# Kernel optimization log

Measured on AMD Instinct MI355X. Metric: run time of the kernel, lower is better.

The kernel has to match this reference:

```python
import jax, jax.numpy as jnp
import numpy as np
from jax import lax

NUM_HEADS = 8
HEAD_DIM = 32  # filters_per_head


def conv1d_same(x, w, b):
    # x: [B, T, Cin], w: [K, Cin, Cout] (WIO), 'same' padding, stride 1
    y = lax.conv_general_dilated(x, w, window_strides=(1,), padding='SAME',
                                 dimension_numbers=('NWC', 'WIO', 'NWC'))
    return y + b


def setup_inputs() -> dict:
    key = jax.random.key(0)
    ks = jax.random.split(key, 9)
    B, T, C = 8, 2048, 256
    K = 3
    s = 1.0 / np.sqrt(K * C)
    return {
        'x': jax.random.normal(ks[0], (B, T, C), dtype=jnp.float32),
        'Wq': jax.random.normal(ks[1], (K, C, C), dtype=jnp.float32) * s,
        'bq': jnp.zeros((C,), dtype=jnp.float32),
        'Wk': jax.random.normal(ks[2], (K, C, C), dtype=jnp.float32) * s,
        'bk': jnp.zeros((C,), dtype=jnp.float32),
        'Wv': jax.random.normal(ks[3], (K, C, C), dtype=jnp.float32) * s,
        'bv': jnp.zeros((C,), dtype=jnp.float32),
        'Wo': jax.random.normal(ks[4], (K, C, C), dtype=jnp.float32) * s,
        'bo': jnp.zeros((C,), dtype=jnp.float32),
    }


def reference(x, Wq, bq, Wk, bk, Wv, bv, Wo, bo):
    B, T, C = x.shape
    q = conv1d_same(x, Wq, bq)
    k = conv1d_same(x, Wk, bk)
    v = conv1d_same(x, Wv, bv)

    def split(t):  # [B, T, C] -> [B, H, T, D]
        return t.reshape(B, T, NUM_HEADS, HEAD_DIM).transpose(0, 2, 1, 3)

    q, k, v = split(q), split(k), split(v)
    scale = 1.0 / jnp.sqrt(jnp.float32(HEAD_DIM))
    logits = jnp.einsum('bhqd,bhkd->bhqk', q, k) * scale  # [B,H,T,T]
    attn = jax.nn.softmax(logits, axis=-1)
    ctx = jnp.einsum('bhqk,bhkd->bhqd', attn, v)
    ctx = ctx.transpose(0, 2, 1, 3).reshape(B, T, C)
    out = x + conv1d_same(ctx, Wo, bo)
    return out
```

## Files before the change

kernel.cpp:

```cpp
#include <hip/hip_runtime.h>
#include <math.h>

#define BDIM 8
#define TDIM 2048
#define CDIM 256
#define HDIM 8
#define DDIM 32
#define TP   (TDIM + 2)

typedef __attribute__((ext_vector_type(8))) short bf16x8;
typedef __attribute__((ext_vector_type(4))) float f32x4;

#if __has_builtin(__builtin_amdgcn_exp2f)
#define EXP2(x) __builtin_amdgcn_exp2f(x)
#else
#define EXP2(x) exp2f(x)
#endif

__device__ __forceinline__ unsigned pk2(float lo, float hi) {
    union { float f; unsigned u; } a, b;
    a.f = lo; b.f = hi;
    return __builtin_amdgcn_perm(b.u + 0x8000u, a.u + 0x8000u, 0x07060302u);
}
__device__ __forceinline__ unsigned pk2t(float lo, float hi) {
    union { float f; unsigned u; } a, b;
    a.f = lo; b.f = hi;
    return __builtin_amdgcn_perm(b.u, a.u, 0x07060302u);
}
__device__ __forceinline__ short bf1(float v) {
    union { float f; unsigned u; } a; a.f = v;
    return (short)((a.u + 0x8000u) >> 16);
}
__device__ __forceinline__ void gld16(const short* g, short* l) {
    __builtin_amdgcn_global_load_lds((const __attribute__((address_space(1))) void*)g,
                                     (__attribute__((address_space(3))) void*)l, 16, 0, 0);
}

#define XBLK 832
#define WBLK 192

__global__ __launch_bounds__(256) void prep_kernel(
    const float* __restrict__ x,
    const float* __restrict__ Wq, const float* __restrict__ Wk,
    const float* __restrict__ Wv, const float* __restrict__ Wo,
    short* __restrict__ xbfp, short* __restrict__ cp,
    short* __restrict__ wcat, short* __restrict__ wot)
{
    const int tid = threadIdx.x;
    if (blockIdx.x < XBLK) {
        const int NX = BDIM * TDIM * 64;
        const int NH = 4096;
        unsigned* xw = (unsigned*)xbfp;
        unsigned* cw = (unsigned*)cp;
        for (int i = blockIdx.x * 256 + tid; i < NX + NH; i += XBLK * 256) {
            if (i < NX) {
                const int bt = i >> 6, c4 = i & 63;
                const int b = bt >> 11, t = bt & 2047;
                const float4 f = *(const float4*)(x + (size_t)bt * 256 + c4 * 4);
                const size_t wo_ = (size_t)(b * TP + t + 1) * 128 + c4 * 2;
                xw[wo_]     = pk2(f.x, f.y);
                xw[wo_ + 1] = pk2(f.z, f.w);
            } else {
                const int hz = i - NX;
                const int half = hz >> 11, z = hz & 2047;
                const int b = z >> 8, r = (z >> 7) & 1, wofs = z & 127;
                const size_t w_ = ((size_t)b * TP + (size_t)r * (TP - 1)) * 128 + wofs;
                if (half == 0) xw[w_] = 0u; else cw[w_] = 0u;
            }
        }
    } else {
        __shared__ float xs[64][65];
        const int wb = blockIdx.x - XBLK;
        const int pair = wb >> 4, sub = wb & 15;
        const int dt = pair >> 2, mat = pair & 3;
        const int ci0 = (sub >> 2) * 64, co0 = (sub & 3) * 64;
        const float* W = mat == 0 ? Wq : mat == 1 ? Wk : mat == 2 ? Wv : Wo;
        const float* src = W + dt * 65536 + (size_t)ci0 * 256 + co0;
        for (int idx = tid; idx < 4096; idx += 256) {
            const int r = idx >> 6, c = idx & 63;
            xs[r][c] = src[(size_t)r * 256 + c];
        }
        __syncthreads();
        short* dstbase = (mat < 3) ? (wcat + (size_t)(mat * 256 + co0) * 768)
                                   : (wot + (size_t)co0 * 768);
        for (int idx = tid; idx < 512; idx += 256) {
            const int co_l = idx >> 3, ci_l = (idx & 7) * 8;
            uint4 u;
            u.x = pk2(xs[ci_l + 0][co_l], xs[ci_l + 1][co_l]);
            u.y = pk2(xs[ci_l + 2][co_l], xs[ci_l + 3][co_l]);
            u.z = pk2(xs[ci_l + 4][co_l], xs[ci_l + 5][co_l]);
            u.w = pk2(xs[ci_l + 6][co_l], xs[ci_l + 7][co_l]);
            *(uint4*)(dstbase + (size_t)co_l * 768 + dt * 256 + ci0 + ci_l) = u;
        }
    }
}

__global__ __launch_bounds__(256) void gemm_qkv(
    const short* __restrict__ xbfp, const short* __restrict__ wcat,
    const float* __restrict__ bq, const float* __restrict__ bk,
    const float* __restrict__ bv,
    short* __restrict__ qo, short* __restrict__ ko, short* __restrict__ vt2)
{
    __shared__ short As[2][4096];
    __shared__ short Bs[2][4096];
    const int tid = threadIdx.x;
    const int wv = tid >> 6, lane = tid & 63, quad = lane >> 4, col = lane & 15;
    const int bx = blockIdx.x;
    const int b = bx >> 4, t0 = (bx & 15) * 128;
    const int by = blockIdx.y;
    const int qkv = by >> 1;
    const int m0 = by * 128;

    const short* wA = wcat + (size_t)m0 * 768;
    const short* xB = xbfp + ((size_t)b * TP + t0) * CDIM;
    const int r0 = tid >> 2, s0 = (tid & 3) * 8;

#define STAGE_Q(kk, bsel) do {                                                  \
    const int dt_ = (kk) >> 3, ci0_ = ((kk) & 7) * 32, k0_ = (kk) * 32;         \
    gld16(wA + (size_t)r0 * 768 + k0_ + s0,        &As[bsel][tid * 8]);         \
    gld16(wA + (size_t)(r0 + 64) * 768 + k0_ + s0, &As[bsel][tid * 8 + 2048]);  \
    gld16(xB + (size_t)(r0 + dt_) * 256 + ci0_ + s0,      &Bs[bsel][tid * 8]);  \
    gld16(xB + (size_t)(r0 + 64 + dt_) * 256 + ci0_ + s0, &Bs[bsel][tid * 8 + 2048]); \
} while (0)

    STAGE_Q(0, 0);

    const float* bias = qkv == 0 ? bq : qkv == 1 ? bk : bv;
    f32x4 acc[4][4];
#pragma unroll
    for (int mt = 0; mt < 4; ++mt) {
        const int cb = ((m0 + (wv & 1) * 64 + mt * 16) & 255) + quad * 4;
        const float4 b4 = *(const float4*)(bias + cb);
#pragma unroll
        for (int nt = 0; nt < 4; ++nt) acc[mt][nt] = (f32x4){b4.x, b4.y, b4.z, b4.w};
    }

    int bsel = 0;
    for (int kk = 0; kk < 24; ++kk) {
        __syncthreads();
        if (kk < 23) STAGE_Q(kk + 1, bsel ^ 1);
        const short* Ab = &As[bsel][((wv & 1) * 64 + col) * 32 + quad * 8];
        const short* Bb = &Bs[bsel][((wv >> 1) * 64 + col) * 32 + quad * 8];
        bf16x8 af[4], bfr[4];
#pragma unroll
        for (int i = 0; i < 4; ++i) {
            af[i]  = *(const bf16x8*)(Ab + i * 512);
            bfr[i] = *(const bf16x8*)(Bb + i * 512);
        }
#pragma unroll
        for (int mt = 0; mt < 4; ++mt)
#pragma unroll
            for (int nt = 0; nt < 4; ++nt)
                acc[mt][nt] = __builtin_amdgcn_mfma_f32_16x16x32_bf16(af[mt], bfr[nt], acc[mt][nt], 0, 0, 0);
        bsel ^= 1;
    }

    const float qs = 0.25503000508221157f;
#pragma unroll
    for (int mt = 0; mt < 4; ++mt) {
        const int cocat = m0 + (wv & 1) * 64 + mt * 16 + quad * 4;
        const int co = cocat & 255;
        const int hh = co >> 5, d = co & 31;
        const size_t bh = (size_t)b * HDIM + hh;
#pragma unroll
        for (int nt = 0; nt < 4; ++nt) {
            const int t = t0 + (wv >> 1) * 64 + nt * 16 + col;
            const f32x4 a = acc[mt][nt];
            if (qkv == 0) {
                uint2 u = make_uint2(pk2(a[0] * qs, a[1] * qs), pk2(a[2] * qs, a[3] * qs));
                *(uint2*)(qo + (bh * TDIM + t) * DDIM + d) = u;
            } else if (qkv == 1) {
                uint2 u = make_uint2(pk2(a[0], a[1]), pk2(a[2], a[3]));
                *(uint2*)(ko + (bh * TDIM + t) * DDIM + d) = u;
            } else {
                const int kt = t >> 6, u6 = t & 63, kg = u6 >> 5, rr = u6 & 31;
                const int j = ((rr >> 4) << 2) | (rr & 3), qd = (rr >> 2) & 3;
                short* vb2 = vt2 + ((bh * 32 + kt) * 2 + kg) * 1024 + qd * 8 + j;
#pragma unroll
                for (int r = 0; r < 4; ++r) vb2[(d + r) * 32] = bf1(a[r]);
            }
        }
    }
#undef STAGE_Q
}

__global__ __launch_bounds__(256) void gemm_res(
    const short* __restrict__ cp, const short* __restrict__ wot,
    const float* __restrict__ bo, const float* __restrict__ x,
    float* __restrict__ out)
{
    __shared__ short As[2][4096];
    __shared__ short Bs[2][4096];
    const int tid = threadIdx.x;
    const int wv = tid >> 6, lane = tid & 63, quad = lane >> 4, col = lane & 15;
    const int bx = blockIdx.x;
    const int b = bx >> 4, t0 = (bx & 15) * 128;
    const int m0 = blockIdx.y * 128;

    const short* wA = wot + (size_t)m0 * 768;
    const short* cB = cp + ((size_t)b * TP + t0) * CDIM;
    const int r0 = tid >> 2, s0 = (tid & 3) * 8;

#define STAGE_R(kk, bsel) do {                                                  \
    const int dt_ = (kk) >> 3, ci0_ = ((kk) & 7) * 32, k0_ = (kk) * 32;         \
    gld16(wA + (size_t)r0 * 768 + k0_ + s0,        &As[bsel][tid * 8]);         \
    gld16(wA + (size_t)(r0 + 64) * 768 + k0_ + s0, &As[bsel][tid * 8 + 2048]);  \
    gld16(cB + (size_t)(r0 + dt_) * 256 + ci0_ + s0,      &Bs[bsel][tid * 8]);  \
    gld16(cB + (size_t)(r0 + 64 + dt_) * 256 + ci0_ + s0, &Bs[bsel][tid * 8 + 2048]); \
} while (0)

    STAGE_R(0, 0);

    f32x4 acc[4][4];
#pragma unroll
    for (int mt = 0; mt < 4; ++mt) {
        const int cb = m0 + (wv & 1) * 64 + mt * 16 + quad * 4;
        const float4 b4 = *(const float4*)(bo + cb);
#pragma unroll
        for (int nt = 0; nt < 4; ++nt) acc[mt][nt] = (f32x4){b4.x, b4.y, b4.z, b4.w};
    }

    int bsel = 0;
    for (int kk = 0; kk < 24; ++kk) {
        __syncthreads();
        if (kk < 23) STAGE_R(kk + 1, bsel ^ 1);
        const short* Ab = &As[bsel][((wv & 1) * 64 + col) * 32 + quad * 8];
        const short* Bb = &Bs[bsel][((wv >> 1) * 64 + col) * 32 + quad * 8];
        bf16x8 af[4], bfr[4];
#pragma unroll
        for (int i = 0; i < 4; ++i) {
            af[i]  = *(const bf16x8*)(Ab + i * 512);
            bfr[i] = *(const bf16x8*)(Bb + i * 512);
        }
#pragma unroll
        for (int mt = 0; mt < 4; ++mt)
#pragma unroll
            for (int nt = 0; nt < 4; ++nt)
                acc[mt][nt] = __builtin_amdgcn_mfma_f32_16x16x32_bf16(af[mt], bfr[nt], acc[mt][nt], 0, 0, 0);
        bsel ^= 1;
    }

#pragma unroll
    for (int mt = 0; mt < 4; ++mt) {
        const int co = m0 + (wv & 1) * 64 + mt * 16 + quad * 4;
#pragma unroll
        for (int nt = 0; nt < 4; ++nt) {
            const int t = t0 + (wv >> 1) * 64 + nt * 16 + col;
            const size_t o = ((size_t)b * TDIM + t) * CDIM + co;
            const float4 xv = *(const float4*)(x + o);
            const f32x4 a = acc[mt][nt];
            *(float4*)(out + o) = make_float4(a[0] + xv.x, a[1] + xv.y, a[2] + xv.z, a[3] + xv.w);
        }
    }
#undef STAGE_R
}

__global__ __launch_bounds__(256, 4) void attn_kernel(
    const short* __restrict__ q, const short* __restrict__ k,
    const short* __restrict__ vt2, short* __restrict__ cp)
{
    __shared__ short ks[2][2048];
    __shared__ short vs[2][2048];
    const int tid = threadIdx.x;
    const int wv = tid >> 6, lane = tid & 63, quad = lane >> 4, col = lane & 15;
    const int bh = blockIdx.x;
    const int q0 = blockIdx.y * 128 + wv * 32;

    const short* qb = q + (size_t)bh * TDIM * DDIM;
    const short* kb = k + (size_t)bh * TDIM * DDIM;
    const short* vb = vt2 + (size_t)bh * TDIM * DDIM;
    const int so = tid * 8;
    const int sw = (tid >> 2) * 32 + (((tid & 3) ^ ((tid >> 3) & 3)) << 3);

    {
        uint4 kr = *(const uint4*)(kb + so);
        uint4 vr = *(const uint4*)(vb + so);
        *(uint4*)&ks[0][sw] = kr;
        *(uint4*)&vs[0][sw] = vr;
    }

    bf16x8 qf[2];
    qf[0] = *(const bf16x8*)(qb + (size_t)(q0 + col) * DDIM + quad * 8);
    qf[1] = *(const bf16x8*)(qb + (size_t)(q0 + 16 + col) * DDIM + quad * 8);

    f32x4 acc0[2] = {{0.f,0.f,0.f,0.f},{0.f,0.f,0.f,0.f}};
    f32x4 acc1[2] = {{0.f,0.f,0.f,0.f},{0.f,0.f,0.f,0.f}};
    f32x4 accl[2] = {{0.f,0.f,0.f,0.f},{0.f,0.f,0.f,0.f}};
    const f32x4 zero = {0.f, 0.f, 0.f, 0.f};
    const short one_bf = (short)0x3F80;
    const bf16x8 ones = {one_bf, one_bf, one_bf, one_bf, one_bf, one_bf, one_bf, one_bf};

    const int foff = col * 32 + ((quad ^ ((col >> 1) & 3)) << 3);
    __syncthreads();

#pragma unroll 2
    for (int kt = 0; kt < TDIM / 64; ++kt) {
        const int cur = kt & 1;
        uint4 krn, vrn;
        const bool more = kt < TDIM / 64 - 1;
        if (more) {
            krn = *(const uint4*)(kb + (kt + 1) * 2048 + so);
            vrn = *(const uint4*)(vb + (kt + 1) * 2048 + so);
        }
        bf16x8 kc[4], vf[4];
#pragma unroll
        for (int g = 0; g < 4; ++g) {
            kc[g] = *(const bf16x8*)&ks[cur][g * 512 + foff];
            vf[g] = *(const bf16x8*)&vs[cur][g * 512 + foff];
        }
#pragma unroll
        for (int qi = 0; qi < 2; ++qi) {
            f32x4 s[4];
            __builtin_amdgcn_s_setprio(1);
#pragma unroll
            for (int g = 0; g < 4; ++g)
                s[g] = __builtin_amdgcn_mfma_f32_16x16x32_bf16(kc[g], qf[qi], zero, 0, 0, 0);
            __builtin_amdgcn_s_setprio(0);
            float p[16];
#pragma unroll
            for (int g = 0; g < 4; ++g)
#pragma unroll
                for (int r = 0; r < 4; ++r)
                    p[g * 4 + r] = EXP2(s[g][r]);
            union { unsigned u[4]; bf16x8 v; } P0, P1;
            P0.u[0] = pk2t(p[0], p[1]);   P0.u[1] = pk2t(p[2], p[3]);
            P0.u[2] = pk2t(p[4], p[5]);   P0.u[3] = pk2t(p[6], p[7]);
            P1.u[0] = pk2t(p[8], p[9]);   P1.u[1] = pk2t(p[10], p[11]);
            P1.u[2] = pk2t(p[12], p[13]); P1.u[3] = pk2t(p[14], p[15]);
            __builtin_amdgcn_s_setprio(1);
            acc0[qi] = __builtin_amdgcn_mfma_f32_16x16x32_bf16(vf[0], P0.v, acc0[qi], 0, 0, 0);
            acc1[qi] = __builtin_amdgcn_mfma_f32_16x16x32_bf16(vf[1], P0.v, acc1[qi], 0, 0, 0);
            accl[qi] = __builtin_amdgcn_mfma_f32_16x16x32_bf16(ones,  P0.v, accl[qi], 0, 0, 0);
            acc0[qi] = __builtin_amdgcn_mfma_f32_16x16x32_bf16(vf[2], P1.v, acc0[qi], 0, 0, 0);
            acc1[qi] = __builtin_amdgcn_mfma_f32_16x16x32_bf16(vf[3], P1.v, acc1[qi], 0, 0, 0);
            accl[qi] = __builtin_amdgcn_mfma_f32_16x16x32_bf16(ones,  P1.v, accl[qi], 0, 0, 0);
            __builtin_amdgcn_s_setprio(0);
        }
        if (more) {
            *(uint4*)&ks[cur ^ 1][sw] = krn;
            *(uint4*)&vs[cur ^ 1][sw] = vrn;
        }
        __syncthreads();
    }

    const int b = bh >> 3, hh = bh & 7;
#pragma unroll
    for (int qi = 0; qi < 2; ++qi) {
        const float inv = 1.f / accl[qi][0];
        const int t = q0 + qi * 16 + col;
        short* crow = cp + ((size_t)b * TP + t + 1) * CDIM + hh * DDIM;
        uint2 u0 = make_uint2(pk2(acc0[qi][0] * inv, acc0[qi][1] * inv),
                              pk2(acc0[qi][2] * inv, acc0[qi][3] * inv));
        uint2 u1 = make_uint2(pk2(acc1[qi][0] * inv, acc1[qi][1] * inv),
                              pk2(acc1[qi][2] * inv, acc1[qi][3] * inv));
        *(uint2*)(crow + quad * 4)      = u0;
        *(uint2*)(crow + 16 + quad * 4) = u1;
    }
}

extern "C" void kernel_launch(void* const* d_in, const int* in_sizes, int n_in,
                              void* d_out, int out_size, void* d_ws, size_t ws_size,
                              hipStream_t stream) {
    const float* x  = (const float*)d_in[0];
    const float* Wq = (const float*)d_in[1];
    const float* bq = (const float*)d_in[2];
    const float* Wk = (const float*)d_in[3];
    const float* bk = (const float*)d_in[4];
    const float* Wv = (const float*)d_in[5];
    const float* bv = (const float*)d_in[6];
    const float* Wo = (const float*)d_in[7];
    const float* bo = (const float*)d_in[8];
    float* out = (float*)d_out;

    short* p = (short*)d_ws;
    short* xbfp = p; p += (size_t)BDIM * TP * CDIM;
    short* cpb  = p; p += (size_t)BDIM * TP * CDIM;
    short* qbuf = p; p += (size_t)BDIM * HDIM * TDIM * DDIM;
    short* kbuf = p; p += (size_t)BDIM * HDIM * TDIM * DDIM;
    short* vt2  = p; p += (size_t)BDIM * HDIM * TDIM * DDIM;
    short* wcat = p; p += 768 * 768;
    short* wot  = p; p += 256 * 768;

    prep_kernel<<<dim3(XBLK + WBLK), 256, 0, stream>>>(x, Wq, Wk, Wv, Wo, xbfp, cpb, wcat, wot);
    gemm_qkv<<<dim3(128, 6), 256, 0, stream>>>(xbfp, wcat, bq, bk, bv, qbuf, kbuf, vt2);
    attn_kernel<<<dim3(64, 16), 256, 0, stream>>>(qbuf, kbuf, vt2, cpb);
    gemm_res<<<dim3(128, 2), 256, 0, stream>>>(cpb, wot, bo, x, out);
}
```

Before: 189.8 us.

## Load K/V fragments directly from global into registers, dropping LDS staging

The attention kernel no longer stages K and V tiles through double-buffered shared memory with block barriers. Each wave now loads its MFMA fragments straight from global memory into registers, prefetching the next tile one iteration ahead, with a wraparound index so the last iteration needs no branch. This removes the LDS writes and reads and the per-tile __syncthreads, at the cost of every wave (four per block) fetching the same K/V data separately. That relies on L1/L2 caching to absorb the duplicated traffic and raises register pressure from the extra prefetch buffers.

```diff
diff --git a/kernel.cpp b/kernel.cpp
--- a/kernel.cpp
+++ b/kernel.cpp
@@ -259,25 +259,15 @@
     const short* __restrict__ q, const short* __restrict__ k,
     const short* __restrict__ vt2, short* __restrict__ cp)
 {
-    __shared__ short ks[2][2048];
-    __shared__ short vs[2][2048];
     const int tid = threadIdx.x;
     const int wv = tid >> 6, lane = tid & 63, quad = lane >> 4, col = lane & 15;
     const int bh = blockIdx.x;
     const int q0 = blockIdx.y * 128 + wv * 32;
 
     const short* qb = q + (size_t)bh * TDIM * DDIM;
-    const short* kb = k + (size_t)bh * TDIM * DDIM;
-    const short* vb = vt2 + (size_t)bh * TDIM * DDIM;
-    const int so = tid * 8;
-    const int sw = (tid >> 2) * 32 + (((tid & 3) ^ ((tid >> 3) & 3)) << 3);
-
-    {
-        uint4 kr = *(const uint4*)(kb + so);
-        uint4 vr = *(const uint4*)(vb + so);
-        *(uint4*)&ks[0][sw] = kr;
-        *(uint4*)&vs[0][sw] = vr;
-    }
+    const int fo = col * 32 + quad * 8;
+    const short* kp = k   + (size_t)bh * TDIM * DDIM + fo;
+    const short* vp = vt2 + (size_t)bh * TDIM * DDIM + fo;
 
     bf16x8 qf[2];
     qf[0] = *(const bf16x8*)(qb + (size_t)(q0 + col) * DDIM + quad * 8);
@@ -290,23 +280,21 @@
     const short one_bf = (short)0x3F80;
     const bf16x8 ones = {one_bf, one_bf, one_bf, one_bf, one_bf, one_bf, one_bf, one_bf};
 
-    const int foff = col * 32 + ((quad ^ ((col >> 1) & 3)) << 3);
-    __syncthreads();
+    bf16x8 kc[4], vf[4];
+#pragma unroll
+    for (int g = 0; g < 4; ++g) {
+        kc[g] = *(const bf16x8*)(kp + g * 512);
+        vf[g] = *(const bf16x8*)(vp + g * 512);
+    }
 
 #pragma unroll 2
     for (int kt = 0; kt < TDIM / 64; ++kt) {
-        const int cur = kt & 1;
-        uint4 krn, vrn;
-        const bool more = kt < TDIM / 64 - 1;
-        if (more) {
-            krn = *(const uint4*)(kb + (kt + 1) * 2048 + so);
-            vrn = *(const uint4*)(vb + (kt + 1) * 2048 + so);
-        }
-        bf16x8 kc[4], vf[4];
+        const int ntile = (kt + 1) & (TDIM / 64 - 1);
+        bf16x8 kn[4], vn[4];
 #pragma unroll
         for (int g = 0; g < 4; ++g) {
-            kc[g] = *(const bf16x8*)&ks[cur][g * 512 + foff];
-            vf[g] = *(const bf16x8*)&vs[cur][g * 512 + foff];
+            kn[g] = *(const bf16x8*)(kp + ntile * 2048 + g * 512);
+            vn[g] = *(const bf16x8*)(vp + ntile * 2048 + g * 512);
         }
 #pragma unroll
         for (int qi = 0; qi < 2; ++qi) {
@@ -336,11 +324,8 @@
             accl[qi] = __builtin_amdgcn_mfma_f32_16x16x32_bf16(ones,  P1.v, accl[qi], 0, 0, 0);
             __builtin_amdgcn_s_setprio(0);
         }
-        if (more) {
-            *(uint4*)&ks[cur ^ 1][sw] = krn;
-            *(uint4*)&vs[cur ^ 1][sw] = vrn;
-        }
-        __syncthreads();
+#pragma unroll
+        for (int g = 0; g < 4; ++g) { kc[g] = kn[g]; vf[g] = vn[g]; }
     }
 
     const int b = bh >> 3, hh = bh & 7;
```

Measured after the change: 202.1 us. 1.06x slower.
